# Kernel tuning notes

Measured on AMD Instinct MI355X. Metric: run time of the kernel, lower is better.

Reference implementation:

```python
import jax, jax.numpy as jnp
import numpy as np

EPS = 1e-05
T_ITERS = 10


def setup_inputs() -> dict:
    key = jax.random.key(0)
    k1, k2 = jax.random.split(key)
    N, C, H, W = 64, 256, 32, 32
    X = jax.random.normal(k1, (N, C, H, W), dtype=jnp.float32)
    # learned rotation matrix (num_groups=1, CxC); random stand-in for the orthogonal matrix
    running_rot = jax.random.normal(k2, (1, C, C), dtype=jnp.float32)
    return {"X": X, "running_rot": running_rot}


def _whiten(X):
    # training-mode whitening: Algorithm 1 (Newton-Schulz iterative ZCA), num_groups=1
    N, C, H, W = X.shape
    g, nc = 1, C
    m = N * H * W
    x = jnp.transpose(X, (1, 0, 2, 3)).reshape(g, nc, m)          # [g, nc, m]
    mean = jnp.mean(x, axis=-1, keepdims=True)
    xc = x - mean
    I = jnp.broadcast_to(jnp.eye(nc, dtype=X.dtype), (g, nc, nc))
    Sigma = EPS * I + jnp.matmul(xc, jnp.swapaxes(xc, 1, 2)) / m  # [g, nc, nc]
    tr_rec = 1.0 / jnp.trace(Sigma, axis1=1, axis2=2)             # [g]
    tr_rec = tr_rec[:, None, None]
    Sigma_N = Sigma * tr_rec
    P = I
    for _ in range(T_ITERS):
        P = 1.5 * P - 0.5 * jnp.matmul(jnp.matmul(jnp.matmul(P, P), P), Sigma_N)
    wm = P * jnp.sqrt(tr_rec)                                     # whitening matrix
    xn = jnp.matmul(wm, xc)                                       # [g, nc, m]
    return jnp.transpose(xn.reshape(C, N, H, W), (1, 0, 2, 3))    # back to NCHW


def reference(X, running_rot):
    N, C, H, W = X.shape
    g, nc = running_rot.shape[0], running_rot.shape[2]
    X_hat = _whiten(X)                                            # [N, C, H, W]
    X_g = X_hat.reshape(N, g, nc, H, W)
    X_rot = jnp.einsum('bgchw,gdc->bgdhw', X_g, running_rot)
    return X_rot.reshape(N, C, H, W)
```

## Files before the change

kernel.cpp:

```cpp
#include <hip/hip_runtime.h>
#include <math.h>

#define C_DIM 256
#define HW_DIM 1024
#define N_DIM 64
#define M_TOTAL (N_DIM * HW_DIM)
#define EPS_F 1e-5f

typedef __attribute__((ext_vector_type(8))) short short8;
typedef __attribute__((ext_vector_type(4))) float v4f;
typedef __attribute__((ext_vector_type(4))) float f4;

union F4S8 { f4 f; short8 s; };
union S8U  { short8 s; unsigned u[4]; };

__device__ __forceinline__ unsigned short f2bf(float x) {
    unsigned u = __float_as_uint(x);
    u = (u + 0x7FFFu + ((u >> 16) & 1u)) >> 16;
    return (unsigned short)u;
}
__device__ __forceinline__ float bf2f(unsigned short h) {
    return __uint_as_float(((unsigned)h) << 16);
}
__device__ __forceinline__ unsigned pack2(float lo, float hi) {
    return (unsigned)f2bf(lo) | ((unsigned)f2bf(hi) << 16);
}
__device__ __forceinline__ void split4v(f4 v, uint2* hi, uint2* lo) {
    unsigned short h0 = f2bf(v[0]), h1 = f2bf(v[1]), h2 = f2bf(v[2]), h3 = f2bf(v[3]);
    float r0 = v[0] - bf2f(h0), r1 = v[1] - bf2f(h1), r2 = v[2] - bf2f(h2), r3 = v[3] - bf2f(h3);
    hi->x = (unsigned)h0 | ((unsigned)h1 << 16);
    hi->y = (unsigned)h2 | ((unsigned)h3 << 16);
    lo->x = (unsigned)f2bf(r0) | ((unsigned)f2bf(r1) << 16);
    lo->y = (unsigned)f2bf(r2) | ((unsigned)f2bf(r3) << 16);
}

__device__ __forceinline__ f4 ldg4_llc(const float* p) {
    f4 v;
    asm volatile("global_load_dwordx4 %0, %1, off sc0 sc1" : "=v"(v) : "v"(p));
    return v;
}
__device__ __forceinline__ short8 ldg8b(const unsigned short* p) {
    F4S8 u; u.f = ldg4_llc((const float*)p); return u.s;
}
__device__ __forceinline__ unsigned ldgus_llc(const unsigned short* p) {
    unsigned v;
    asm volatile("global_load_ushort %0, %1, off sc0 sc1" : "=v"(v) : "v"(p));
    return v;
}
__device__ __forceinline__ void stgus_llc(unsigned short* p, unsigned v) {
    asm volatile("global_store_short %0, %1, off sc0 sc1" :: "v"(p), "v"(v));
}
__device__ __forceinline__ void vm_wait0() {
    asm volatile("s_waitcnt vmcnt(0)" ::: "memory");
    __builtin_amdgcn_sched_barrier(0);
}

__device__ __forceinline__ void gsync(unsigned* bar, unsigned target) {
    asm volatile("s_waitcnt vmcnt(0)" ::: "memory");
    __syncthreads();
    if (threadIdx.x == 0) {
        __hip_atomic_fetch_add(bar, 1u, __ATOMIC_RELAXED, __HIP_MEMORY_SCOPE_AGENT);
        while (__hip_atomic_load(bar, __ATOMIC_RELAXED, __HIP_MEMORY_SCOPE_AGENT) < target)
            __builtin_amdgcn_s_sleep(1);
    }
    __syncthreads();
}

__global__ void prepass_kernel(const float* __restrict__ X, unsigned short* __restrict__ Xbf,
                               float* __restrict__ musum) {
    int b = blockIdx.x;
    int t = threadIdx.x;
    int r = t >> 6;
    int l = t & 63;
    size_t row = (size_t)(4 * b + r);
    const float4* src = (const float4*)(X + (row << 10));
    uint2* dst = (uint2*)(Xbf + (row << 10));
    float s = 0.f;
#pragma unroll
    for (int j = 0; j < 4; ++j) {
        float4 v = src[l + 64 * j];
        uint2 p; p.x = pack2(v.x, v.y); p.y = pack2(v.z, v.w);
        dst[l + 64 * j] = p;
        s += v.x + v.y + v.z + v.w;
    }
    for (int off = 32; off > 0; off >>= 1) s += __shfl_down(s, off);
    if (l == 0) atomicAdd(&musum[(4 * b + r) & 255], s);
}

__global__ __launch_bounds__(512, 3)
void gram_mfma(const unsigned short* __restrict__ Xbf, float* __restrict__ G) {
    int tile = blockIdx.x;
    int ci = (tile >> 1) * 128;
    int cj = (tile == 0) ? 0 : 128;
    int ks = blockIdx.y;
    int t = threadIdx.x, wave = t >> 6, lane = t & 63;
    int wy = wave >> 2, wx = wave & 3;
    int quad = lane >> 4, l16 = lane & 15;

    __shared__ __align__(16) unsigned short As[128 * 72];
    __shared__ __align__(16) unsigned short Bs[128 * 72];
    const unsigned short* Bsrc = (ci == cj) ? As : Bs;

    v4f acc[4][2] = {};
    int n = ks >> 1;
    int hwbase = (ks & 1) * 512;
    const unsigned short* base = Xbf + (((size_t)n * C_DIM) << 10);
    int srow = t >> 2;
    int schunk = t & 3;

    for (int s = 0; s < 8; ++s) {
        int k0 = hwbase + s * 64;
        __syncthreads();
#pragma unroll
        for (int h = 0; h < 2; ++h) {
            int ch = schunk + 4 * h;
            *(uint4*)&As[srow * 72 + ch * 8] =
                *(const uint4*)&base[(((size_t)(ci + srow)) << 10) + k0 + ch * 8];
            if (ci != cj)
                *(uint4*)&Bs[srow * 72 + ch * 8] =
                    *(const uint4*)&base[(((size_t)(cj + srow)) << 10) + k0 + ch * 8];
        }
        __syncthreads();

        short8 af[4][2], bfr[2][2];
#pragma unroll
        for (int mt = 0; mt < 4; ++mt)
#pragma unroll
            for (int kh = 0; kh < 2; ++kh)
                af[mt][kh] = *(const short8*)&As[(64 * wy + 16 * mt + l16) * 72 + kh * 32 + quad * 8];
#pragma unroll
        for (int nt = 0; nt < 2; ++nt)
#pragma unroll
            for (int kh = 0; kh < 2; ++kh)
                bfr[nt][kh] = *(const short8*)&Bsrc[(32 * wx + 16 * nt + l16) * 72 + kh * 32 + quad * 8];
#pragma unroll
        for (int kh = 0; kh < 2; ++kh)
#pragma unroll
            for (int mt = 0; mt < 4; ++mt)
#pragma unroll
                for (int nt = 0; nt < 2; ++nt)
                    acc[mt][nt] = __builtin_amdgcn_mfma_f32_16x16x32_bf16(af[mt][kh], bfr[nt][kh], acc[mt][nt], 0, 0, 0);
    }

#pragma unroll
    for (int mt = 0; mt < 4; ++mt)
#pragma unroll
        for (int nt = 0; nt < 2; ++nt)
#pragma unroll
            for (int r = 0; r < 4; ++r) {
                int row = ci + 64 * wy + 16 * mt + 4 * quad + r;
                int col = cj + 32 * wx + 16 * nt + l16;
                atomicAdd(&G[row * C_DIM + col], acc[mt][nt][r]);
            }
}

__global__ __launch_bounds__(256, 1)
void ns_persist(const float* __restrict__ G, const float* __restrict__ musum,
                const float* __restrict__ R,
                unsigned short* Ph, unsigned short* Pl,
                unsigned short* Sh, unsigned short* Sl,
                unsigned short* T1h, unsigned short* T1l,
                unsigned short* T2h, unsigned short* T2l,
                unsigned short* __restrict__ Mbf, float* __restrict__ moff,
                unsigned* bar) {
    __shared__ float part[4 * 512];
    __shared__ float red[256];
    __shared__ float scal_sh[2];

    int bid = blockIdx.x;
    int t = threadIdx.x;
    int wv = t >> 6, lane = t & 63;
    int quad = lane >> 4, l16 = lane & 15;
    int kb = wv * 64;
    unsigned tg = 0;

    {
        float mu = musum[t] * (1.0f / M_TOTAL);
        float d = G[t * (C_DIM + 1)] * (1.0f / M_TOTAL) - mu * mu + EPS_F;
        red[t] = d;
        __syncthreads();
        for (int off = 128; off > 0; off >>= 1) {
            if (t < off) red[t] += red[t + off];
            __syncthreads();
        }
        if (t == 0) {
            float trr = 1.0f / red[0];
            scal_sh[0] = trr;
            scal_sh[1] = sqrtf(trr);
        }
        __syncthreads();
    }
    float trr = scal_sh[0];
    float s1  = scal_sh[1];

    {
        int idx = bid * 256 + t;
        int r = idx >> 8, c = idx & 255;
        float g = (r >= 128 && c < 128) ? G[c * C_DIM + r] : G[idx];
        float mu_r = musum[r] * (1.0f / M_TOTAL);
        float mu_c = musum[c] * (1.0f / M_TOTAL);
        float sig = (g * (1.0f / M_TOTAL) - mu_r * mu_c + ((r == c) ? EPS_F : 0.f)) * trr;
        float p0  = ((r == c) ? 1.5f : 0.f) - 0.5f * sig;
        unsigned short sh_ = f2bf(sig);
        unsigned short sl_ = f2bf(sig - bf2f(sh_));
        unsigned short ph_ = f2bf(p0);
        unsigned short pl_ = f2bf(p0 - bf2f(ph_));
        stgus_llc(&Sh[idx], sh_); stgus_llc(&Sl[idx], sl_);
        stgus_llc(&Ph[idx], ph_); stgus_llc(&Pl[idx], pl_);
    }
    tg += 256; gsync(bar, tg);

    for (int it = 1; it < 10; ++it) {
        {
            bool isT2 = (bid >= 128);
            int b = bid & 127;
            int ci = (b >> 4) * 32, cj = (b & 15) * 16;
            const unsigned short* Bh_ = isT2 ? Sh : Ph;
            const unsigned short* Bl_ = isT2 ? Sl : Pl;
            unsigned short* Dh = isT2 ? T2h : T1h;
            unsigned short* Dl = isT2 ? T2l : T1l;

            short8 ah[2][2], al[2][2], bh[2], bl[2];
#pragma unroll
            for (int mt = 0; mt < 2; ++mt)
#pragma unroll
                for (int ks = 0; ks < 2; ++ks) {
                    int off = (ci + 16 * mt + l16) * C_DIM + kb + 32 * ks + 8 * quad;
                    ah[mt][ks] = ldg8b(&Ph[off]);
                    al[mt][ks] = ldg8b(&Pl[off]);
                }
#pragma unroll
            for (int ks = 0; ks < 2; ++ks) {
                int off = (cj + l16) * C_DIM + kb + 32 * ks + 8 * quad;
                bh[ks] = ldg8b(&Bh_[off]);
                bl[ks] = ldg8b(&Bl_[off]);
            }
            vm_wait0();
            v4f acc[2] = {};
#pragma unroll
            for (int ks = 0; ks < 2; ++ks)
#pragma unroll
                for (int mt = 0; mt < 2; ++mt) {
                    acc[mt] = __builtin_amdgcn_mfma_f32_16x16x32_bf16(ah[mt][ks], bh[ks], acc[mt], 0, 0, 0);
                    acc[mt] = __builtin_amdgcn_mfma_f32_16x16x32_bf16(ah[mt][ks], bl[ks], acc[mt], 0, 0, 0);
                    acc[mt] = __builtin_amdgcn_mfma_f32_16x16x32_bf16(al[mt][ks], bh[ks], acc[mt], 0, 0, 0);
                }
#pragma unroll
            for (int mt = 0; mt < 2; ++mt)
#pragma unroll
                for (int r = 0; r < 4; ++r)
                    part[wv * 512 + (16 * mt + 4 * quad + r) * 16 + l16] = acc[mt][r];
            __syncthreads();
#pragma unroll
            for (int e = 0; e < 512; e += 256) {
                int ee = e + t;
                float v = part[ee] + part[512 + ee] + part[1024 + ee] + part[1536 + ee];
                int row = ee >> 4, col = ee & 15;
                unsigned short h = f2bf(v);
                unsigned short lo2 = f2bf(v - bf2f(h));
                int gidx = (ci + row) * C_DIM + cj + col;
                stgus_llc(&Dh[gidx], h);
                stgus_llc(&Dl[gidx], lo2);
            }
        }
        tg += 256; gsync(bar, tg);
        {
            int ci = (bid >> 4) * 16, cj = (bid & 15) * 16;
            short8 ah[2], al[2], bh[2], bl[2];
#pragma unroll
            for (int ks = 0; ks < 2; ++ks) {
                int offa = (ci + l16) * C_DIM + kb + 32 * ks + 8 * quad;
                int offb = (cj + l16) * C_DIM + kb + 32 * ks + 8 * quad;
                ah[ks] = ldg8b(&T1h[offa]);
                al[ks] = ldg8b(&T1l[offa]);
                bh[ks] = ldg8b(&T2h[offb]);
                bl[ks] = ldg8b(&T2l[offb]);
            }
            vm_wait0();
            v4f acc = {};
#pragma unroll
            for (int ks = 0; ks < 2; ++ks) {
                acc = __builtin_amdgcn_mfma_f32_16x16x32_bf16(ah[ks], bh[ks], acc, 0, 0, 0);
                acc = __builtin_amdgcn_mfma_f32_16x16x32_bf16(ah[ks], bl[ks], acc, 0, 0, 0);
                acc = __builtin_amdgcn_mfma_f32_16x16x32_bf16(al[ks], bh[ks], acc, 0, 0, 0);
            }
#pragma unroll
            for (int r = 0; r < 4; ++r)
                part[wv * 256 + (4 * quad + r) * 16 + l16] = acc[r];
            __syncthreads();
            {
                float u = part[t] + part[256 + t] + part[512 + t] + part[768 + t];
                int row = t >> 4, col = t & 15;
                int gidx = (ci + row) * C_DIM + cj + col;
                unsigned hu = ldgus_llc(&Ph[gidx]);
                unsigned lu = ldgus_llc(&Pl[gidx]);
                vm_wait0();
                float p = bf2f((unsigned short)hu) + bf2f((unsigned short)lu);
                float v = 1.5f * p - 0.5f * u;
                unsigned short h = f2bf(v);
                unsigned short lo2 = f2bf(v - bf2f(h));
                stgus_llc(&Ph[gidx], h);
                stgus_llc(&Pl[gidx], lo2);
            }
        }
        tg += 256; gsync(bar, tg);
    }

    {
        int ci = (bid >> 4) * 16, cj = (bid & 15) * 16;
        short8 rh[2], rl[2], bh[2], bl[2];
#pragma unroll
        for (int ks = 0; ks < 2; ++ks) {
            const float* rp = &R[(ci + l16) * C_DIM + kb + 32 * ks + 8 * quad];
            f4 a0 = *(const f4*)rp;
            f4 a1 = *(const f4*)(rp + 4);
            uint2 h0, l0, h1, l1;
            split4v(a0, &h0, &l0);
            split4v(a1, &h1, &l1);
            S8U sh_; sh_.u[0] = h0.x; sh_.u[1] = h0.y; sh_.u[2] = h1.x; sh_.u[3] = h1.y;
            S8U sl_; sl_.u[0] = l0.x; sl_.u[1] = l0.y; sl_.u[2] = l1.x; sl_.u[3] = l1.y;
            rh[ks] = sh_.s;
            rl[ks] = sl_.s;
            int offb = (cj + l16) * C_DIM + kb + 32 * ks + 8 * quad;
            bh[ks] = ldg8b(&Ph[offb]);
            bl[ks] = ldg8b(&Pl[offb]);
        }
        vm_wait0();
        v4f acc = {};
#pragma unroll
        for (int ks = 0; ks < 2; ++ks) {
            acc = __builtin_amdgcn_mfma_f32_16x16x32_bf16(rh[ks], bh[ks], acc, 0, 0, 0);
            acc = __builtin_amdgcn_mfma_f32_16x16x32_bf16(rh[ks], bl[ks], acc, 0, 0, 0);
            acc = __builtin_amdgcn_mfma_f32_16x16x32_bf16(rl[ks], bh[ks], acc, 0, 0, 0);
        }
#pragma unroll
        for (int r = 0; r < 4; ++r)
            part[wv * 256 + (4 * quad + r) * 16 + l16] = acc[r];
        __syncthreads();
        float u = part[t] + part[256 + t] + part[512 + t] + part[768 + t];
        int row = t >> 4, col = t & 15;
        float val = u * s1;
        Mbf[(ci + row) * C_DIM + cj + col] = f2bf(val);
        float contrib = val * (musum[cj + col] * (1.0f / M_TOTAL));
        __syncthreads();
        part[t] = contrib;
        __syncthreads();
        if ((t & 15) == 0) {
            float s = 0.f;
#pragma unroll
            for (int i = 0; i < 16; ++i) s += part[t + i];
            atomicAdd(&moff[ci + (t >> 4)], s);
        }
    }
}

__global__ void out_mfma(const unsigned short* __restrict__ Xbf,
                         const unsigned short* __restrict__ Mbf,
                         const float* __restrict__ moff, float* __restrict__ out) {
    int hwb = blockIdx.x * 128;
    int db  = blockIdx.y * 128;
    int n   = blockIdx.z;
    int t = threadIdx.x, wave = t >> 6, lane = t & 63;
    int wy = wave >> 1, wx = wave & 1, quad = lane >> 4, l16 = lane & 15;

    __shared__ __align__(16) unsigned short Asm[128 * 40];
    __shared__ __align__(16) unsigned short Bsm[128 * 34];
    __shared__ __align__(16) float Ep[4 * 16 * 68];

    v4f acc[4][4] = {};
    const unsigned short* Xn = Xbf + (((size_t)n * C_DIM) << 10);

    for (int kb = 0; kb < 256; kb += 32) {
        __syncthreads();
#pragma unroll
        for (int i = 0; i < 2; ++i) {
            int a = t + 256 * i;
            int row = a >> 2, c8 = a & 3;
            *(uint4*)(&Asm[row * 40 + 8 * c8]) =
                *(const uint4*)(&Mbf[(db + row) * C_DIM + kb + 8 * c8]);
        }
#pragma unroll
        for (int i = 0; i < 16; ++i) {
            int idx = t + 256 * i;
            int hw = idx & 127, crow = idx >> 7;
            Bsm[hw * 34 + crow] = Xn[(((size_t)(kb + crow)) << 10) + hwb + hw];
        }
        __syncthreads();

        short8 af[4], bfr[4];
#pragma unroll
        for (int mt = 0; mt < 4; ++mt)
            af[mt] = *(const short8*)(&Asm[(64 * wy + 16 * mt + l16) * 40 + 8 * quad]);
#pragma unroll
        for (int nt = 0; nt < 4; ++nt) {
            union { short8 s; unsigned u[4]; } tmp;
            const unsigned short* bp = &Bsm[(64 * wx + 16 * nt + l16) * 34 + 8 * quad];
            tmp.u[0] = *(const unsigned*)(bp + 0);
            tmp.u[1] = *(const unsigned*)(bp + 2);
            tmp.u[2] = *(const unsigned*)(bp + 4);
            tmp.u[3] = *(const unsigned*)(bp + 6);
            bfr[nt] = tmp.s;
        }
#pragma unroll
        for (int mt = 0; mt < 4; ++mt)
#pragma unroll
            for (int nt = 0; nt < 4; ++nt)
                acc[mt][nt] = __builtin_amdgcn_mfma_f32_16x16x32_bf16(af[mt], bfr[nt], acc[mt][nt], 0, 0, 0);
    }

    float* W = &Ep[wave * 16 * 68];
#pragma unroll
    for (int mt = 0; mt < 4; ++mt) {
#pragma unroll
        for (int r = 0; r < 4; ++r) {
            float off = moff[db + 64 * wy + 16 * mt + 4 * quad + r];
#pragma unroll
            for (int nt = 0; nt < 4; ++nt)
                W[(4 * quad + r) * 68 + 16 * nt + l16] = acc[mt][nt][r] - off;
        }
        __syncthreads();
#pragma unroll
        for (int j = 0; j < 4; ++j) {
            int row = 4 * j + quad;
            float4 v = *(const float4*)&W[row * 68 + 4 * l16];
            int d = db + 64 * wy + 16 * mt + row;
            int hw = hwb + 64 * wx + 4 * l16;
            *(float4*)&out[(((size_t)(n * C_DIM + d)) << 10) + hw] = v;
        }
        __syncthreads();
    }
}

extern "C" void kernel_launch(void* const* d_in, const int* in_sizes, int n_in,
                              void* d_out, int out_size, void* d_ws, size_t ws_size,
                              hipStream_t stream) {
    const float* X = (const float*)d_in[0];
    const float* R = (const float*)d_in[1];
    float* out = (float*)d_out;
    float* ws  = (float*)d_ws;

    float* musum = ws;
    unsigned* bar = (unsigned*)(ws + 256);
    float* moff  = ws + 272;
    float* G     = ws + 528;
    unsigned short* Ph  = (unsigned short*)(G + 65536);
    unsigned short* Pl  = Ph  + 65536;
    unsigned short* Sh  = Pl  + 65536;
    unsigned short* Sl  = Sh  + 65536;
    unsigned short* T1h = Sl  + 65536;
    unsigned short* T1l = T1h + 65536;
    unsigned short* T2h = T1l + 65536;
    unsigned short* T2l = T2h + 65536;
    unsigned short* Mbf = T2l + 65536;
    unsigned short* Xbf = Mbf + 65536;

    hipMemsetAsync(ws, 0, (528 + 65536) * sizeof(float), stream);

    prepass_kernel<<<4096, 256, 0, stream>>>(X, Xbf, musum);
    gram_mfma<<<dim3(3, 128), 512, 0, stream>>>(Xbf, G);

    ns_persist<<<256, 256, 0, stream>>>(G, musum, R, Ph, Pl, Sh, Sl,
                                        T1h, T1l, T2h, T2l, Mbf, moff, bar);

    out_mfma<<<dim3(8, 2, 64), 256, 0, stream>>>(Xbf, Mbf, moff, out);
}
```

Baseline: 346.1 us.

## Use two-level tree grid barrier and widen output GEMM tile to all channels

The grid barrier in the persistent Newton-Schulz kernel now uses 16 leaf counters on separate 128-byte lines plus a root counter, instead of all 256 blocks hammering one atomic, to reduce contention at each of the ~19 syncs. The output GEMM now computes all 256 output channels per block (8x4 MFMA tiles per wave), so each X tile is loaded into LDS once rather than twice. This doubles accumulator registers and A-tile LDS and halves the number of blocks, which may lower occupancy.

```diff
diff --git a/kernel.cpp b/kernel.cpp
--- a/kernel.cpp
+++ b/kernel.cpp
@@ -55,12 +55,16 @@
     __builtin_amdgcn_sched_barrier(0);
 }
 
-__device__ __forceinline__ void gsync(unsigned* bar, unsigned target) {
+__device__ __forceinline__ void gsync(unsigned* bar, int bid, unsigned p) {
     asm volatile("s_waitcnt vmcnt(0)" ::: "memory");
     __syncthreads();
     if (threadIdx.x == 0) {
-        __hip_atomic_fetch_add(bar, 1u, __ATOMIC_RELAXED, __HIP_MEMORY_SCOPE_AGENT);
-        while (__hip_atomic_load(bar, __ATOMIC_RELAXED, __HIP_MEMORY_SCOPE_AGENT) < target)
+        unsigned* leaf = bar + ((unsigned)(bid & 15)) * 32;
+        unsigned* root = bar + 16 * 32;
+        unsigned prev = __hip_atomic_fetch_add(leaf, 1u, __ATOMIC_RELAXED, __HIP_MEMORY_SCOPE_AGENT);
+        if (prev == 16u * p - 1u)
+            __hip_atomic_fetch_add(root, 1u, __ATOMIC_RELAXED, __HIP_MEMORY_SCOPE_AGENT);
+        while (__hip_atomic_load(root, __ATOMIC_RELAXED, __HIP_MEMORY_SCOPE_AGENT) < 16u * p)
             __builtin_amdgcn_s_sleep(1);
     }
     __syncthreads();
@@ -172,7 +176,7 @@
     int wv = t >> 6, lane = t & 63;
     int quad = lane >> 4, l16 = lane & 15;
     int kb = wv * 64;
-    unsigned tg = 0;
+    unsigned ph = 0;
 
     {
         float mu = musum[t] * (1.0f / M_TOTAL);
@@ -208,7 +212,7 @@
         stgus_llc(&Sh[idx], sh_); stgus_llc(&Sl[idx], sl_);
         stgus_llc(&Ph[idx], ph_); stgus_llc(&Pl[idx], pl_);
     }
-    tg += 256; gsync(bar, tg);
+    ++ph; gsync(bar, bid, ph);
 
     for (int it = 1; it < 10; ++it) {
         {
@@ -263,7 +267,7 @@
                 stgus_llc(&Dl[gidx], lo2);
             }
         }
-        tg += 256; gsync(bar, tg);
+        ++ph; gsync(bar, bid, ph);
         {
             int ci = (bid >> 4) * 16, cj = (bid & 15) * 16;
             short8 ah[2], al[2], bh[2], bl[2];
@@ -303,7 +307,7 @@
                 stgus_llc(&Pl[gidx], lo2);
             }
         }
-        tg += 256; gsync(bar, tg);
+        ++ph; gsync(bar, bid, ph);
     }
 
     {
@@ -354,30 +358,30 @@
     }
 }
 
-__global__ void out_mfma(const unsigned short* __restrict__ Xbf,
-                         const unsigned short* __restrict__ Mbf,
-                         const float* __restrict__ moff, float* __restrict__ out) {
+__global__ __launch_bounds__(256)
+void out_mfma(const unsigned short* __restrict__ Xbf,
+              const unsigned short* __restrict__ Mbf,
+              const float* __restrict__ moff, float* __restrict__ out) {
     int hwb = blockIdx.x * 128;
-    int db  = blockIdx.y * 128;
-    int n   = blockIdx.z;
+    int n   = blockIdx.y;
     int t = threadIdx.x, wave = t >> 6, lane = t & 63;
     int wy = wave >> 1, wx = wave & 1, quad = lane >> 4, l16 = lane & 15;
 
-    __shared__ __align__(16) unsigned short Asm[128 * 40];
+    __shared__ __align__(16) unsigned short Asm[256 * 40];
     __shared__ __align__(16) unsigned short Bsm[128 * 34];
     __shared__ __align__(16) float Ep[4 * 16 * 68];
 
-    v4f acc[4][4] = {};
+    v4f acc[8][4] = {};
     const unsigned short* Xn = Xbf + (((size_t)n * C_DIM) << 10);
 
     for (int kb = 0; kb < 256; kb += 32) {
         __syncthreads();
 #pragma unroll
-        for (int i = 0; i < 2; ++i) {
+        for (int i = 0; i < 4; ++i) {
             int a = t + 256 * i;
             int row = a >> 2, c8 = a & 3;
             *(uint4*)(&Asm[row * 40 + 8 * c8]) =
-                *(const uint4*)(&Mbf[(db + row) * C_DIM + kb + 8 * c8]);
+                *(const uint4*)(&Mbf[row * C_DIM + kb + 8 * c8]);
         }
 #pragma unroll
         for (int i = 0; i < 16; ++i) {
@@ -387,10 +391,10 @@
         }
         __syncthreads();
 
-        short8 af[4], bfr[4];
-#pragma unroll
-        for (int mt = 0; mt < 4; ++mt)
-            af[mt] = *(const short8*)(&Asm[(64 * wy + 16 * mt + l16) * 40 + 8 * quad]);
+        short8 af[8], bfr[4];
+#pragma unroll
+        for (int mt = 0; mt < 8; ++mt)
+            af[mt] = *(const short8*)(&Asm[(128 * wy + 16 * mt + l16) * 40 + 8 * quad]);
 #pragma unroll
         for (int nt = 0; nt < 4; ++nt) {
             union { short8 s; unsigned u[4]; } tmp;
@@ -402,7 +406,7 @@
             bfr[nt] = tmp.s;
         }
 #pragma unroll
-        for (int mt = 0; mt < 4; ++mt)
+        for (int mt = 0; mt < 8; ++mt)
 #pragma unroll
             for (int nt = 0; nt < 4; ++nt)
                 acc[mt][nt] = __builtin_amdgcn_mfma_f32_16x16x32_bf16(af[mt], bfr[nt], acc[mt][nt], 0, 0, 0);
@@ -410,10 +414,10 @@
 
     float* W = &Ep[wave * 16 * 68];
 #pragma unroll
-    for (int mt = 0; mt < 4; ++mt) {
+    for (int mt = 0; mt < 8; ++mt) {
 #pragma unroll
         for (int r = 0; r < 4; ++r) {
-            float off = moff[db + 64 * wy + 16 * mt + 4 * quad + r];
+            float off = moff[128 * wy + 16 * mt + 4 * quad + r];
 #pragma unroll
             for (int nt = 0; nt < 4; ++nt)
                 W[(4 * quad + r) * 68 + 16 * nt + l16] = acc[mt][nt][r] - off;
@@ -423,7 +427,7 @@
         for (int j = 0; j < 4; ++j) {
             int row = 4 * j + quad;
             float4 v = *(const float4*)&W[row * 68 + 4 * l16];
-            int d = db + 64 * wy + 16 * mt + row;
+            int d = 128 * wy + 16 * mt + row;
             int hw = hwb + 64 * wx + 4 * l16;
             *(float4*)&out[(((size_t)(n * C_DIM + d)) << 10) + hw] = v;
         }
@@ -440,9 +444,9 @@
     float* ws  = (float*)d_ws;
 
     float* musum = ws;
-    unsigned* bar = (unsigned*)(ws + 256);
-    float* moff  = ws + 272;
-    float* G     = ws + 528;
+    float* moff  = ws + 256;
+    unsigned* bar = (unsigned*)(ws + 512);
+    float* G     = ws + 1088;
     unsigned short* Ph  = (unsigned short*)(G + 65536);
     unsigned short* Pl  = Ph  + 65536;
     unsigned short* Sh  = Pl  + 65536;
@@ -454,7 +458,7 @@
     unsigned short* Mbf = T2l + 65536;
     unsigned short* Xbf = Mbf + 65536;
 
-    hipMemsetAsync(ws, 0, (528 + 65536) * sizeof(float), stream);
+    hipMemsetAsync(ws, 0, (1088 + 65536) * sizeof(float), stream);
 
     prepass_kernel<<<4096, 256, 0, stream>>>(X, Xbf, musum);
     gram_mfma<<<dim3(3, 128), 512, 0, stream>>>(Xbf, G);
@@ -462,5 +466,5 @@
     ns_persist<<<256, 256, 0, stream>>>(G, musum, R, Ph, Pl, Sh, Sl,
                                         T1h, T1l, T2h, T2l, Mbf, moff, bar);
 
-    out_mfma<<<dim3(8, 2, 64), 256, 0, stream>>>(Xbf, Mbf, moff, out);
-}
+    out_mfma<<<dim3(8, 64), 256, 0, stream>>>(Xbf, Mbf, moff, out);
+}
```

Measured after the change: 281.6 us. 18.6% less time.
